# Optimization experiments

Measured on AMD Instinct MI355X. Metric: run time of the kernel, lower is better.

Reference implementation:

```python
import jax, jax.numpy as jnp
import numpy as np
from jax import lax

EPS = 0.05 ** 2        # geomloss: eps = blur**p with p=2
N_ITERS = 50           # fixed log-domain Sinkhorn iterations (converged regime)
W_MSE = 1.0
W_OT = 1.0


def _sqcost(x, y):
    # x: (B,T,C), y: (B,S,C) -> (B,T,S) cost C_ij = 0.5*||x_i - y_j||^2
    x2 = jnp.sum(x * x, axis=-1)                      # (B,T)
    y2 = jnp.sum(y * y, axis=-1)                      # (B,S)
    xy = jnp.einsum('btc,bsc->bts', x, y)             # (B,T,S)
    return 0.5 * (x2[:, :, None] + y2[:, None, :] - 2.0 * xy)


def _softmin(C, h, logw):
    # -eps * logsumexp_j( logw + (h_j - C_ij)/eps );  C:(B,T,S), h:(B,S) -> (B,T)
    return -EPS * jax.nn.logsumexp(logw + (h[:, None, :] - C) / EPS, axis=-1)


def _sinkhorn_divergence(x, y):
    # Debiased entropic Sinkhorn divergence with uniform weights, per batch. (B,)
    B, T, _ = x.shape
    S = y.shape[1]
    loga = -np.float32(np.log(T))
    logb = -np.float32(np.log(S))
    C_xy = _sqcost(x, y)          # (B,T,S)
    C_xx = _sqcost(x, x)          # (B,T,T)
    C_yy = _sqcost(y, y)          # (B,S,S)
    C_yx = jnp.swapaxes(C_xy, 1, 2)

    f = jnp.zeros((B, T), x.dtype)   # potential on x for OT(x,y)
    g = jnp.zeros((B, S), x.dtype)   # potential on y for OT(x,y)
    p = jnp.zeros((B, T), x.dtype)   # symmetric potential for OT(x,x)
    q = jnp.zeros((B, S), x.dtype)   # symmetric potential for OT(y,y)

    @jax.checkpoint
    def step(carry, _):
        f, g, p, q = carry
        f1 = _softmin(C_xy, g, logb)
        g1 = _softmin(C_yx, f, loga)
        p1 = _softmin(C_xx, p, loga)
        q1 = _softmin(C_yy, q, logb)
        # averaged (stabilized) updates, as in geomloss symmetric Sinkhorn
        return (0.5 * (f + f1), 0.5 * (g + g1), 0.5 * (p + p1), 0.5 * (q + q1)), None

    (f, g, p, q), _ = lax.scan(step, (f, g, p, q), None, length=N_ITERS)
    # S_eps(a,b) = <a, f - p> + <b, g - q>  with uniform a, b
    return jnp.mean(f - p, axis=1) + jnp.mean(g - q, axis=1)


def setup_inputs() -> dict:
    key = jax.random.key(0)
    k1, k2 = jax.random.split(key)
    B, T, C = 8, 1024, 16
    pred = jax.random.normal(k1, (B, T, C), dtype=jnp.float32)
    gt = jax.random.normal(k2, (B, T, C), dtype=jnp.float32)
    return {"pred_sequence": pred, "gt_sequence": gt}


def reference(pred_sequence, gt_sequence):
    mse_loss = jnp.mean((pred_sequence - gt_sequence) ** 2)
    ot_loss = jnp.mean(_sinkhorn_divergence(pred_sequence, gt_sequence))
    total = W_MSE * mse_loss + W_OT * ot_loss
    return jnp.stack([total, mse_loss, ot_loss])  # (total, mse, ot)
```

## Files before the change

### kernel.cpp

```cpp
#include <hip/hip_runtime.h>
#include <hip/hip_fp16.h>

#define NN 1024
#define BATCH 8
#define CDIM 16
#define NITER 36
#define CAPC 512
#define CAPF 256

static constexpr float K_SCALE = 577.0780163555854f;
static constexpr float EPS_LN2 = 0.0017328679513998632f;
static constexpr float MARGIN_T = 1.1f * 577.0780163555854f;
static constexpr float MARGIN_C = 4.0f * 577.0780163555854f;

#if __has_builtin(__builtin_amdgcn_exp2f)
#define EXP2F(x) __builtin_amdgcn_exp2f(x)
#else
#define EXP2F(x) exp2f(x)
#endif
#if __has_builtin(__builtin_amdgcn_logf)
#define LOG2F(x) __builtin_amdgcn_logf(x)
#else
#define LOG2F(x) log2f(x)
#endif

#if __has_builtin(__builtin_amdgcn_mfma_f32_16x16x16f16)
#define HAVE_MFMA16 1
using f16x4 = __attribute__((ext_vector_type(4))) _Float16;
using f32x4 = __attribute__((ext_vector_type(4))) float;
#endif

__device__ float g_pot[2][4][BATCH][NN];
__device__ float g_mse_part[8];
__device__ __align__(16) unsigned g_cand_c[4 * BATCH * NN * CAPC];
__device__ unsigned g_cnt_c[4 * BATCH * NN];
__device__ __align__(16) unsigned g_cand_f[4 * BATCH * NN * CAPF];
__device__ unsigned g_cnt_f[4 * BATCH * NN];

struct alignas(8) H4 { __half2 a, b; };

__device__ inline float2 cvt2(unsigned int u) {
    __half2 h;
    *reinterpret_cast<unsigned int*>(&h) = u;
    return __half22float2(h);
}

__global__ __launch_bounds__(512) void cost_t0_kernel(const float* __restrict__ x,
                                                      const float* __restrict__ y) {
    int bid = blockIdx.x;
    int m = bid >> 9;
    int b = (bid >> 6) & 7;
    int ig = bid & 63;
    const float* X = (m == 1 || m == 3) ? y : x;
    const float* Y = (m == 0 || m == 3) ? y : x;
    int tid = threadIdx.x;
    int lane = tid & 63, wid = tid >> 6;

    __shared__ __align__(16) __half tile[16][NN];
    __shared__ __align__(16) float xs[16 * CDIM];
    __shared__ __align__(16) float x2s[16];

    if (tid < 16 * CDIM) xs[tid] = X[(size_t)(b * NN + ig * 16) * CDIM + tid];
    __syncthreads();
    if (tid < 16) {
        float a = 0.0f;
        #pragma unroll
        for (int k = 0; k < CDIM; ++k) a = fmaf(xs[tid * CDIM + k], xs[tid * CDIM + k], a);
        x2s[tid] = 0.5f * a;
    }
    __syncthreads();

#if HAVE_MFMA16
    {
        int arow = lane & 15;
        int kb = (lane >> 4) * 4;
        f16x4 af;
        af[0] = (_Float16)(-xs[arow * CDIM + kb + 0]);
        af[1] = (_Float16)(-xs[arow * CDIM + kb + 1]);
        af[2] = (_Float16)(-xs[arow * CDIM + kb + 2]);
        af[3] = (_Float16)(-xs[arow * CDIM + kb + 3]);
        float4 xq = reinterpret_cast<const float4*>(x2s)[lane >> 4];
        int r0 = (lane >> 4) * 4;
        int cb = lane & 15;

        #pragma unroll 1
        for (int s2 = 0; s2 < 8; ++s2) {
            int col = wid * 128 + s2 * 16 + cb;
            float4 bv = *reinterpret_cast<const float4*>(
                Y + (size_t)(b * NN + col) * CDIM + (lane >> 4) * 4);
            float p = bv.x * bv.x + bv.y * bv.y + bv.z * bv.z + bv.w * bv.w;
            p += __shfl_xor(p, 16, 64);
            p += __shfl_xor(p, 32, 64);
            float y2c = 0.5f * p;
            f16x4 bf;
            bf[0] = (_Float16)bv.x; bf[1] = (_Float16)bv.y;
            bf[2] = (_Float16)bv.z; bf[3] = (_Float16)bv.w;
            f32x4 cin;
            cin[0] = xq.x + y2c; cin[1] = xq.y + y2c;
            cin[2] = xq.z + y2c; cin[3] = xq.w + y2c;
            f32x4 d = __builtin_amdgcn_mfma_f32_16x16x16f16(af, bf, cin, 0, 0, 0);
            #pragma unroll
            for (int r = 0; r < 4; ++r)
                tile[r0 + r][col] = __float2half_rn(d[r]);
        }
    }
#else
    {
        int j0 = tid * 2;
        float yr[2][16];
        const float4* Y4 = reinterpret_cast<const float4*>(Y + (size_t)(b * NN + j0) * CDIM);
        #pragma unroll
        for (int rr = 0; rr < 2; ++rr) {
            #pragma unroll
            for (int q = 0; q < 4; ++q) {
                float4 v = Y4[rr * 4 + q];
                yr[rr][q * 4 + 0] = v.x; yr[rr][q * 4 + 1] = v.y;
                yr[rr][q * 4 + 2] = v.z; yr[rr][q * 4 + 3] = v.w;
            }
        }
        float y2h[2];
        #pragma unroll
        for (int rr = 0; rr < 2; ++rr) {
            float acc = 0.0f;
            #pragma unroll
            for (int k = 0; k < CDIM; ++k) acc = fmaf(yr[rr][k], yr[rr][k], acc);
            y2h[rr] = 0.5f * acc;
        }
        #pragma unroll 1
        for (int r = 0; r < 16; ++r) {
            float xv[CDIM];
            #pragma unroll
            for (int k = 0; k < CDIM; ++k) xv[k] = xs[r * CDIM + k];
            float x2h = x2s[r];
            float acc[2];
            #pragma unroll
            for (int rr = 0; rr < 2; ++rr) {
                float a = x2h + y2h[rr];
                #pragma unroll
                for (int k = 0; k < CDIM; ++k) a = fmaf(xv[k], -yr[rr][k], a);
                acc[rr] = a;
            }
            *reinterpret_cast<__half2*>(&tile[r][j0]) = __floats2half2_rn(acc[0], acc[1]);
        }
    }
#endif
    __syncthreads();

    #pragma unroll 1
    for (int r = 0; r < 2; ++r) {
        int rloc = wid * 2 + r;
        int i = ig * 16 + rloc;
        const uint4* crow = reinterpret_cast<const uint4*>(&tile[rloc][0]);
        uint4 ca = crow[lane];
        uint4 cb = crow[64 + lane];

        float t[16];
        {
            float2 f;
            f = cvt2(ca.x); t[0] = f.x * -K_SCALE;  t[1] = f.y * -K_SCALE;
            f = cvt2(ca.y); t[2] = f.x * -K_SCALE;  t[3] = f.y * -K_SCALE;
            f = cvt2(ca.z); t[4] = f.x * -K_SCALE;  t[5] = f.y * -K_SCALE;
            f = cvt2(ca.w); t[6] = f.x * -K_SCALE;  t[7] = f.y * -K_SCALE;
            f = cvt2(cb.x); t[8] = f.x * -K_SCALE;  t[9] = f.y * -K_SCALE;
            f = cvt2(cb.y); t[10] = f.x * -K_SCALE; t[11] = f.y * -K_SCALE;
            f = cvt2(cb.z); t[12] = f.x * -K_SCALE; t[13] = f.y * -K_SCALE;
            f = cvt2(cb.w); t[14] = f.x * -K_SCALE; t[15] = f.y * -K_SCALE;
        }

        float mx = t[0];
        #pragma unroll
        for (int k = 1; k < 16; ++k) mx = fmaxf(mx, t[k]);
        #pragma unroll
        for (int off = 32; off; off >>= 1) mx = fmaxf(mx, __shfl_xor(mx, off, 64));

        float s = 0.0f;
        #pragma unroll
        for (int k = 0; k < 16; ++k) s += EXP2F(t[k] - mx);
        #pragma unroll
        for (int off = 32; off; off >>= 1) s += __shfl_xor(s, off, 64);

        if (lane == 0) {
            float res = -EPS_LN2 * (mx - 10.0f + LOG2F(s));
            g_pot[1][m][b][i] = 0.5f * res;
        }

        size_t rowid = (size_t)((m * BATCH + b) * NN + i);
        float thr = mx - MARGIN_C;
        int c = 0;
        #pragma unroll
        for (int k = 0; k < 16; ++k) c += (t[k] >= thr) ? 1 : 0;
        int incl = c;
        #pragma unroll
        for (int off = 1; off < 64; off <<= 1) {
            int v = __shfl_up(incl, off, 64);
            if (lane >= off) incl += v;
        }
        int excl = incl - c;
        int total = __shfl(incl, 63, 64);
        if (lane == 0) g_cnt_c[rowid] = (unsigned)(total < CAPC ? total : CAPC);

        union U4 { uint4 q; unsigned w[4]; } A, B2;
        A.q = ca; B2.q = cb;
        unsigned* dst = &g_cand_c[rowid * CAPC];
        int slot = excl;
        #pragma unroll
        for (int k = 0; k < 16; ++k) {
            if (t[k] >= thr) {
                if (slot < CAPC) {
                    unsigned hb = (k < 8) ? A.w[k >> 1] : B2.w[(k - 8) >> 1];
                    hb = (hb >> ((k & 1) * 16)) & 0xffffu;
                    unsigned j = (k < 8) ? (unsigned)(lane * 8 + k)
                                         : (unsigned)(512 + lane * 8 + (k - 8));
                    dst[slot] = (j << 16) | hb;
                }
                ++slot;
            }
        }
    }

    if (m == 0 && ig == 0) {
        const float4* xa = reinterpret_cast<const float4*>(x + (size_t)b * NN * CDIM);
        const float4* ya = reinterpret_cast<const float4*>(y + (size_t)b * NN * CDIM);
        float acc = 0.0f;
        for (int e = tid; e < NN * CDIM / 4; e += 512) {
            float4 xv = xa[e], yv = ya[e];
            float d0 = xv.x - yv.x, d1 = xv.y - yv.y;
            float d2 = xv.z - yv.z, d3 = xv.w - yv.w;
            acc = fmaf(d0, d0, acc); acc = fmaf(d1, d1, acc);
            acc = fmaf(d2, d2, acc); acc = fmaf(d3, d3, acc);
        }
        #pragma unroll
        for (int off = 32; off; off >>= 1) acc += __shfl_xor(acc, off, 64);
        __shared__ float red[8];
        if (lane == 0) red[wid] = acc;
        __syncthreads();
        if (tid == 0) {
            float r2 = 0.0f;
            #pragma unroll
            for (int w = 0; w < 8; ++w) r2 += red[w];
            g_mse_part[b] = r2;
        }
    }
}

template <bool BUILDF, bool COARSE_SRC>
__global__ __launch_bounds__(256) void sparse_iter_t(int parity) {
    int bid = blockIdx.x;
    int p = bid >> 7;
    int b = (bid >> 4) & 7;
    int rg = bid & 15;
    int hsel = (p == 0) ? 1 : (p == 1) ? 0 : p;

    const float* __restrict__ hin  = g_pot[parity][hsel][b];
    const float* __restrict__ oldp = g_pot[parity][p][b];
    float* __restrict__ outp       = g_pot[parity ^ 1][p][b];

    __shared__ float h2[NN];
    {
        const float4* h4 = reinterpret_cast<const float4*>(hin);
        float4 v = h4[threadIdx.x];
        v.x *= K_SCALE; v.y *= K_SCALE; v.z *= K_SCALE; v.w *= K_SCALE;
        reinterpret_cast<float4*>(h2)[threadIdx.x] = v;
    }
    __syncthreads();

    int tid = threadIdx.x;
    int lane = tid & 63, wid = tid >> 6;
    int c = lane & 3;
    int i = rg * 64 + wid * 16 + (lane >> 2);
    size_t rowid = (size_t)((p * BATCH + b) * NN + i);

    const unsigned* __restrict__ candsrc = COARSE_SRC ? g_cand_c : g_cand_f;
    const int cap = COARSE_SRC ? CAPC : CAPF;
    int cnt = (int)(COARSE_SRC ? g_cnt_c[rowid] : g_cnt_f[rowid]);
    const uint4* __restrict__ cd4 =
        reinterpret_cast<const uint4*>(candsrc + rowid * cap);

    float m = -3.0e38f;
    float s = 0.0f;
    int nstep = (cnt + 15) >> 4;
    for (int k = 0; k < nstep; ++k) {
        int base = k * 16 + c * 4;
        uint4 u = cd4[k * 4 + c];
        __half hh;
        *reinterpret_cast<unsigned short*>(&hh) = (unsigned short)(u.x & 0xffffu);
        float t0 = fmaf(__half2float(hh), -K_SCALE, h2[(u.x >> 16) & 1023]);
        *reinterpret_cast<unsigned short*>(&hh) = (unsigned short)(u.y & 0xffffu);
        float t1 = fmaf(__half2float(hh), -K_SCALE, h2[(u.y >> 16) & 1023]);
        *reinterpret_cast<unsigned short*>(&hh) = (unsigned short)(u.z & 0xffffu);
        float t2 = fmaf(__half2float(hh), -K_SCALE, h2[(u.z >> 16) & 1023]);
        *reinterpret_cast<unsigned short*>(&hh) = (unsigned short)(u.w & 0xffffu);
        float t3 = fmaf(__half2float(hh), -K_SCALE, h2[(u.w >> 16) & 1023]);
        t0 = (base + 0 < cnt) ? t0 : -3.0e38f;
        t1 = (base + 1 < cnt) ? t1 : -3.0e38f;
        t2 = (base + 2 < cnt) ? t2 : -3.0e38f;
        t3 = (base + 3 < cnt) ? t3 : -3.0e38f;
        float sm = fmaxf(fmaxf(t0, t1), fmaxf(t2, t3));
        float nm = fmaxf(m, sm);
        s = s * EXP2F(m - nm) + EXP2F(t0 - nm) + EXP2F(t1 - nm)
                              + EXP2F(t2 - nm) + EXP2F(t3 - nm);
        m = nm;
    }
    #pragma unroll
    for (int off = 1; off <= 2; off <<= 1) {
        float m2 = __shfl_xor(m, off, 64);
        float s2 = __shfl_xor(s, off, 64);
        float nm = fmaxf(m, m2);
        s = s * EXP2F(m - nm) + s2 * EXP2F(m2 - nm);
        m = nm;
    }
    if (c == 0) {
        float res = -EPS_LN2 * (m - 10.0f + LOG2F(s));
        outp[i] = 0.5f * (oldp[i] + res);
    }

    if (BUILDF) {
        float thr = m - MARGIN_T;
        int cl = 0;
        for (int k = 0; k < nstep; ++k) {
            int base = k * 16 + c * 4;
            uint4 u = cd4[k * 4 + c];
            unsigned w[4] = {u.x, u.y, u.z, u.w};
            #pragma unroll
            for (int o = 0; o < 4; ++o) {
                if (base + o < cnt) {
                    __half hh;
                    *reinterpret_cast<unsigned short*>(&hh) = (unsigned short)(w[o] & 0xffffu);
                    float tv = fmaf(__half2float(hh), -K_SCALE, h2[(w[o] >> 16) & 1023]);
                    if (tv >= thr) ++cl;
                }
            }
        }
        int g0 = lane & ~3;
        int c0 = __shfl(cl, g0 + 0, 64);
        int c1 = __shfl(cl, g0 + 1, 64);
        int c2 = __shfl(cl, g0 + 2, 64);
        int c3 = __shfl(cl, g0 + 3, 64);
        int excl = ((c >= 1) ? c0 : 0) + ((c >= 2) ? c1 : 0) + ((c >= 3) ? c2 : 0);
        int total = c0 + c1 + c2 + c3;
        if (c == 0) g_cnt_f[rowid] = (unsigned)(total < CAPF ? total : CAPF);
        unsigned* dst = &g_cand_f[rowid * CAPF];
        int slot = excl;
        for (int k = 0; k < nstep; ++k) {
            int base = k * 16 + c * 4;
            uint4 u = cd4[k * 4 + c];
            unsigned w[4] = {u.x, u.y, u.z, u.w};
            #pragma unroll
            for (int o = 0; o < 4; ++o) {
                if (base + o < cnt) {
                    __half hh;
                    *reinterpret_cast<unsigned short*>(&hh) = (unsigned short)(w[o] & 0xffffu);
                    float tv = fmaf(__half2float(hh), -K_SCALE, h2[(w[o] >> 16) & 1023]);
                    if (tv >= thr) {
                        if (slot < CAPF) dst[slot] = w[o];
                        ++slot;
                    }
                }
            }
        }
    }
}

__global__ __launch_bounds__(256) void epilogue_kernel(float* __restrict__ out) {
    int tid = threadIdx.x;
    const float* f = &g_pot[0][0][0][0];
    const float* g = &g_pot[0][1][0][0];
    const float* pp = &g_pot[0][2][0][0];
    const float* q = &g_pot[0][3][0][0];
    float acc = 0.0f;
    for (int idx = tid; idx < BATCH * NN; idx += 256) {
        acc += (f[idx] - pp[idx]) + (g[idx] - q[idx]);
    }
    float macc = (tid < 8) ? g_mse_part[tid] : 0.0f;
    #pragma unroll
    for (int off = 32; off; off >>= 1) {
        acc += __shfl_xor(acc, off, 64);
        macc += __shfl_xor(macc, off, 64);
    }
    __shared__ float red[4], redm[4];
    int lane = tid & 63, wid = tid >> 6;
    if (lane == 0) { red[wid] = acc; redm[wid] = macc; }
    __syncthreads();
    if (tid == 0) {
        float ot = (red[0] + red[1] + red[2] + red[3]) / (float)(BATCH * NN);
        float mse = (redm[0] + redm[1] + redm[2] + redm[3]) / (float)(BATCH * NN * CDIM);
        out[0] = mse + ot;
        out[1] = mse;
        out[2] = ot;
    }
}

extern "C" void kernel_launch(void* const* d_in, const int* in_sizes, int n_in,
                              void* d_out, int out_size, void* d_ws, size_t ws_size,
                              hipStream_t stream) {
    const float* pred = (const float*)d_in[0];
    const float* gt   = (const float*)d_in[1];
    float* out = (float*)d_out;

    cost_t0_kernel<<<4 * BATCH * 64, 512, 0, stream>>>(pred, gt);
    sparse_iter_t<false, true><<<512, 256, 0, stream>>>(1);
    sparse_iter_t<true, true><<<512, 256, 0, stream>>>(0);
    for (int t = 3; t < NITER; ++t) {
        sparse_iter_t<false, false><<<512, 256, 0, stream>>>(t & 1);
    }
    epilogue_kernel<<<1, 256, 0, stream>>>(out);
}
```

Baseline: 158.4 us.

## Keep MFMA cost tiles in registers and compact candidates via shared atomics

The first-iteration cost kernel no longer writes the fp16 cost tile to shared memory and re-reads it per row. Row max and sum reductions now run directly on MFMA accumulator registers through cross-lane shuffles and per-wave shared partials. Candidate compaction uses a shared-memory atomic counter per row in place of a wave prefix scan. Candidate order inside each row now depends on atomic arrival order, the row max is taken from fp32 values rather than rounded fp16, and contention on 16 shared counters may serialize.

```diff
diff --git a/kernel.cpp b/kernel.cpp
--- a/kernel.cpp
+++ b/kernel.cpp
@@ -26,9 +26,9 @@
 
 #if __has_builtin(__builtin_amdgcn_mfma_f32_16x16x16f16)
 #define HAVE_MFMA16 1
+#endif
 using f16x4 = __attribute__((ext_vector_type(4))) _Float16;
 using f32x4 = __attribute__((ext_vector_type(4))) float;
-#endif
 
 __device__ float g_pot[2][4][BATCH][NN];
 __device__ float g_mse_part[8];
@@ -36,8 +36,6 @@
 __device__ unsigned g_cnt_c[4 * BATCH * NN];
 __device__ __align__(16) unsigned g_cand_f[4 * BATCH * NN * CAPF];
 __device__ unsigned g_cnt_f[4 * BATCH * NN];
-
-struct alignas(8) H4 { __half2 a, b; };
 
 __device__ inline float2 cvt2(unsigned int u) {
     __half2 h;
@@ -56,11 +54,14 @@
     int tid = threadIdx.x;
     int lane = tid & 63, wid = tid >> 6;
 
-    __shared__ __align__(16) __half tile[16][NN];
     __shared__ __align__(16) float xs[16 * CDIM];
     __shared__ __align__(16) float x2s[16];
+    __shared__ float wms[16][8];
+    __shared__ float wss[16][8];
+    __shared__ int scnt[16];
 
     if (tid < 16 * CDIM) xs[tid] = X[(size_t)(b * NN + ig * 16) * CDIM + tid];
+    if (tid < 16) scnt[tid] = 0;
     __syncthreads();
     if (tid < 16) {
         float a = 0.0f;
@@ -70,24 +71,25 @@
     }
     __syncthreads();
 
+    int r0 = (lane >> 4) * 4;
+    int cb = lane & 15;
+    int kb = (lane >> 4) * 4;
+    float4 xq = reinterpret_cast<const float4*>(x2s)[lane >> 4];
+
+    f32x4 dv[8];
 #if HAVE_MFMA16
     {
         int arow = lane & 15;
-        int kb = (lane >> 4) * 4;
         f16x4 af;
         af[0] = (_Float16)(-xs[arow * CDIM + kb + 0]);
         af[1] = (_Float16)(-xs[arow * CDIM + kb + 1]);
         af[2] = (_Float16)(-xs[arow * CDIM + kb + 2]);
         af[3] = (_Float16)(-xs[arow * CDIM + kb + 3]);
-        float4 xq = reinterpret_cast<const float4*>(x2s)[lane >> 4];
-        int r0 = (lane >> 4) * 4;
-        int cb = lane & 15;
-
         #pragma unroll 1
         for (int s2 = 0; s2 < 8; ++s2) {
             int col = wid * 128 + s2 * 16 + cb;
             float4 bv = *reinterpret_cast<const float4*>(
-                Y + (size_t)(b * NN + col) * CDIM + (lane >> 4) * 4);
+                Y + (size_t)(b * NN + col) * CDIM + kb);
             float p = bv.x * bv.x + bv.y * bv.y + bv.z * bv.z + bv.w * bv.w;
             p += __shfl_xor(p, 16, 64);
             p += __shfl_xor(p, 32, 64);
@@ -98,123 +100,116 @@
             f32x4 cin;
             cin[0] = xq.x + y2c; cin[1] = xq.y + y2c;
             cin[2] = xq.z + y2c; cin[3] = xq.w + y2c;
-            f32x4 d = __builtin_amdgcn_mfma_f32_16x16x16f16(af, bf, cin, 0, 0, 0);
-            #pragma unroll
-            for (int r = 0; r < 4; ++r)
-                tile[r0 + r][col] = __float2half_rn(d[r]);
+            dv[s2] = __builtin_amdgcn_mfma_f32_16x16x16f16(af, bf, cin, 0, 0, 0);
         }
     }
 #else
     {
-        int j0 = tid * 2;
-        float yr[2][16];
-        const float4* Y4 = reinterpret_cast<const float4*>(Y + (size_t)(b * NN + j0) * CDIM);
-        #pragma unroll
-        for (int rr = 0; rr < 2; ++rr) {
+        #pragma unroll 1
+        for (int s2 = 0; s2 < 8; ++s2) {
+            int col = wid * 128 + s2 * 16 + cb;
+            float yv[16];
+            const float4* Yc = reinterpret_cast<const float4*>(Y + (size_t)(b * NN + col) * CDIM);
             #pragma unroll
             for (int q = 0; q < 4; ++q) {
-                float4 v = Y4[rr * 4 + q];
-                yr[rr][q * 4 + 0] = v.x; yr[rr][q * 4 + 1] = v.y;
-                yr[rr][q * 4 + 2] = v.z; yr[rr][q * 4 + 3] = v.w;
+                float4 v = Yc[q];
+                yv[q * 4 + 0] = v.x; yv[q * 4 + 1] = v.y;
+                yv[q * 4 + 2] = v.z; yv[q * 4 + 3] = v.w;
             }
-        }
-        float y2h[2];
-        #pragma unroll
-        for (int rr = 0; rr < 2; ++rr) {
-            float acc = 0.0f;
-            #pragma unroll
-            for (int k = 0; k < CDIM; ++k) acc = fmaf(yr[rr][k], yr[rr][k], acc);
-            y2h[rr] = 0.5f * acc;
-        }
-        #pragma unroll 1
-        for (int r = 0; r < 16; ++r) {
-            float xv[CDIM];
-            #pragma unroll
-            for (int k = 0; k < CDIM; ++k) xv[k] = xs[r * CDIM + k];
-            float x2h = x2s[r];
-            float acc[2];
-            #pragma unroll
-            for (int rr = 0; rr < 2; ++rr) {
-                float a = x2h + y2h[rr];
+            float y2c = 0.0f;
+            #pragma unroll
+            for (int k = 0; k < 16; ++k) y2c = fmaf(yv[k], yv[k], y2c);
+            y2c *= 0.5f;
+            #pragma unroll
+            for (int r = 0; r < 4; ++r) {
+                float a = ((const float*)&xq)[r] + y2c;
                 #pragma unroll
-                for (int k = 0; k < CDIM; ++k) a = fmaf(xv[k], -yr[rr][k], a);
-                acc[rr] = a;
+                for (int k = 0; k < 16; ++k)
+                    a = fmaf(xs[(r0 + r) * CDIM + k], -yv[k], a);
+                dv[s2][r] = a;
             }
-            *reinterpret_cast<__half2*>(&tile[r][j0]) = __floats2half2_rn(acc[0], acc[1]);
         }
     }
 #endif
-    __syncthreads();
+
+    float mnr[4];
+    #pragma unroll
+    for (int r = 0; r < 4; ++r) {
+        float v = dv[0][r];
+        #pragma unroll
+        for (int s2 = 1; s2 < 8; ++s2) v = fminf(v, dv[s2][r]);
+        mnr[r] = v;
+    }
+    #pragma unroll
+    for (int off = 1; off <= 8; off <<= 1) {
+        #pragma unroll
+        for (int r = 0; r < 4; ++r) mnr[r] = fminf(mnr[r], __shfl_xor(mnr[r], off, 64));
+    }
+    if ((lane & 15) == 0) {
+        #pragma unroll
+        for (int r = 0; r < 4; ++r) wms[r0 + r][wid] = mnr[r];
+    }
+    __syncthreads();
+
+    float bmx[4];
+    #pragma unroll
+    for (int r = 0; r < 4; ++r) {
+        float v = wms[r0 + r][0];
+        #pragma unroll
+        for (int w = 1; w < 8; ++w) v = fminf(v, wms[r0 + r][w]);
+        bmx[r] = v * -K_SCALE;
+    }
+
+    size_t rowbase = (size_t)((m * BATCH + b) * NN + ig * 16);
+    float sr[4];
+    #pragma unroll
+    for (int r = 0; r < 4; ++r) {
+        float s = 0.0f;
+        #pragma unroll
+        for (int s2 = 0; s2 < 8; ++s2)
+            s += EXP2F(fmaf(dv[s2][r], -K_SCALE, -bmx[r]));
+        sr[r] = s;
+    }
+    #pragma unroll
+    for (int off = 1; off <= 8; off <<= 1) {
+        #pragma unroll
+        for (int r = 0; r < 4; ++r) sr[r] += __shfl_xor(sr[r], off, 64);
+    }
+    if ((lane & 15) == 0) {
+        #pragma unroll
+        for (int r = 0; r < 4; ++r) wss[r0 + r][wid] = sr[r];
+    }
 
     #pragma unroll 1
-    for (int r = 0; r < 2; ++r) {
-        int rloc = wid * 2 + r;
-        int i = ig * 16 + rloc;
-        const uint4* crow = reinterpret_cast<const uint4*>(&tile[rloc][0]);
-        uint4 ca = crow[lane];
-        uint4 cb = crow[64 + lane];
-
-        float t[16];
-        {
-            float2 f;
-            f = cvt2(ca.x); t[0] = f.x * -K_SCALE;  t[1] = f.y * -K_SCALE;
-            f = cvt2(ca.y); t[2] = f.x * -K_SCALE;  t[3] = f.y * -K_SCALE;
-            f = cvt2(ca.z); t[4] = f.x * -K_SCALE;  t[5] = f.y * -K_SCALE;
-            f = cvt2(ca.w); t[6] = f.x * -K_SCALE;  t[7] = f.y * -K_SCALE;
-            f = cvt2(cb.x); t[8] = f.x * -K_SCALE;  t[9] = f.y * -K_SCALE;
-            f = cvt2(cb.y); t[10] = f.x * -K_SCALE; t[11] = f.y * -K_SCALE;
-            f = cvt2(cb.z); t[12] = f.x * -K_SCALE; t[13] = f.y * -K_SCALE;
-            f = cvt2(cb.w); t[14] = f.x * -K_SCALE; t[15] = f.y * -K_SCALE;
-        }
-
-        float mx = t[0];
-        #pragma unroll
-        for (int k = 1; k < 16; ++k) mx = fmaxf(mx, t[k]);
-        #pragma unroll
-        for (int off = 32; off; off >>= 1) mx = fmaxf(mx, __shfl_xor(mx, off, 64));
-
-        float s = 0.0f;
-        #pragma unroll
-        for (int k = 0; k < 16; ++k) s += EXP2F(t[k] - mx);
-        #pragma unroll
-        for (int off = 32; off; off >>= 1) s += __shfl_xor(s, off, 64);
-
-        if (lane == 0) {
-            float res = -EPS_LN2 * (mx - 10.0f + LOG2F(s));
-            g_pot[1][m][b][i] = 0.5f * res;
-        }
-
-        size_t rowid = (size_t)((m * BATCH + b) * NN + i);
-        float thr = mx - MARGIN_C;
-        int c = 0;
-        #pragma unroll
-        for (int k = 0; k < 16; ++k) c += (t[k] >= thr) ? 1 : 0;
-        int incl = c;
-        #pragma unroll
-        for (int off = 1; off < 64; off <<= 1) {
-            int v = __shfl_up(incl, off, 64);
-            if (lane >= off) incl += v;
-        }
-        int excl = incl - c;
-        int total = __shfl(incl, 63, 64);
-        if (lane == 0) g_cnt_c[rowid] = (unsigned)(total < CAPC ? total : CAPC);
-
-        union U4 { uint4 q; unsigned w[4]; } A, B2;
-        A.q = ca; B2.q = cb;
-        unsigned* dst = &g_cand_c[rowid * CAPC];
-        int slot = excl;
-        #pragma unroll
-        for (int k = 0; k < 16; ++k) {
-            if (t[k] >= thr) {
+    for (int s2 = 0; s2 < 8; ++s2) {
+        int col = wid * 128 + s2 * 16 + cb;
+        #pragma unroll
+        for (int r = 0; r < 4; ++r) {
+            float tv = dv[s2][r] * -K_SCALE;
+            if (tv >= bmx[r] - MARGIN_C) {
+                int slot = atomicAdd(&scnt[r0 + r], 1);
                 if (slot < CAPC) {
-                    unsigned hb = (k < 8) ? A.w[k >> 1] : B2.w[(k - 8) >> 1];
-                    hb = (hb >> ((k & 1) * 16)) & 0xffffu;
-                    unsigned j = (k < 8) ? (unsigned)(lane * 8 + k)
-                                         : (unsigned)(512 + lane * 8 + (k - 8));
-                    dst[slot] = (j << 16) | hb;
+                    union { __half h; unsigned short u; } cvt;
+                    cvt.h = __float2half_rn(dv[s2][r]);
+                    g_cand_c[(rowbase + r0 + r) * CAPC + slot] =
+                        ((unsigned)col << 16) | (unsigned)cvt.u;
                 }
-                ++slot;
             }
+        }
+    }
+    __syncthreads();
+
+    if (wid == 0 && (lane & 15) == 0) {
+        #pragma unroll
+        for (int r = 0; r < 4; ++r) {
+            int rr = r0 + r;
+            float stot = 0.0f;
+            #pragma unroll
+            for (int w = 0; w < 8; ++w) stot += wss[rr][w];
+            float res = -EPS_LN2 * (bmx[r] - 10.0f + LOG2F(stot));
+            g_pot[1][m][b][ig * 16 + rr] = 0.5f * res;
+            int cc = scnt[rr];
+            g_cnt_c[rowbase + rr] = (unsigned)(cc < CAPC ? cc : CAPC);
         }
     }
 
```

Result: no change. 157.1 us (-0.8%).
